# Kernel tuning notes

Hardware: AMD Instinct MI355X
Metric: run time of the kernel (lower is better)

Reference implementation:

```python
import jax, jax.numpy as jnp
import numpy as np

B, C_IMG, H, W = 16, 512, 32, 32
C_AUD, K_LEN, N_HEADS = 512, 256, 8
HEAD_DIM = C_AUD // N_HEADS
EPS = 1e-5


def setup_inputs() -> dict:
    key = jax.random.key(0)
    ks = jax.random.split(key, 12)
    s_img = 1.0 / np.sqrt(C_IMG)
    s_aud = 1.0 / np.sqrt(C_AUD)
    return {
        "img_feat": jax.random.normal(ks[0], (B, C_IMG, H, W), jnp.float32),
        "audio_feat": jax.random.normal(ks[1], (B, K_LEN, C_AUD), jnp.float32),
        "Wq": jax.random.uniform(ks[2], (C_IMG, C_AUD), jnp.float32, -s_img, s_img),
        "bq": jnp.zeros((C_AUD,), jnp.float32),
        "Wk": jax.random.uniform(ks[3], (C_AUD, C_AUD), jnp.float32, -s_aud, s_aud),
        "bk": jnp.zeros((C_AUD,), jnp.float32),
        "Wv": jax.random.uniform(ks[4], (C_AUD, C_AUD), jnp.float32, -s_aud, s_aud),
        "bv": jnp.zeros((C_AUD,), jnp.float32),
        "Wo": jax.random.uniform(ks[5], (C_AUD, C_IMG), jnp.float32, -s_aud, s_aud),
        "bo": jnp.zeros((C_IMG,), jnp.float32),
        "gamma": jnp.ones((C_IMG,), jnp.float32),
        "beta": jnp.zeros((C_IMG,), jnp.float32),
    }


def reference(img_feat, audio_feat, Wq, bq, Wk, bk, Wv, bv, Wo, bo, gamma, beta):
    b, c, h, w = img_feat.shape
    # b c h w -> b (h w) c
    img_seq = img_feat.reshape(b, c, h * w).transpose(0, 2, 1)
    q = img_seq @ Wq + bq                      # [b, q, C_AUD]
    k = audio_feat @ Wk + bk                   # [b, k, C_AUD]
    v = audio_feat @ Wv + bv
    # split heads: b s (h d) -> b h s d
    def split(x):
        bs, s, _ = x.shape
        return x.reshape(bs, s, N_HEADS, HEAD_DIM).transpose(0, 2, 1, 3)
    qh, kh, vh = split(q), split(k), split(v)
    scale = HEAD_DIM ** -0.5
    scores = jnp.einsum('bhqd,bhkd->bhqk', qh, kh) * scale
    weights = jax.nn.softmax(scores, axis=-1)
    attn = jnp.einsum('bhqk,bhkd->bhqd', weights, vh)
    attn = attn.transpose(0, 2, 1, 3).reshape(b, h * w, C_AUD)
    proj = attn @ Wo + bo                      # [b, q, C_IMG]
    y = img_seq + proj
    mu = jnp.mean(y, axis=-1, keepdims=True)
    var = jnp.mean((y - mu) ** 2, axis=-1, keepdims=True)
    y = (y - mu) * jax.lax.rsqrt(var + EPS) * gamma + beta
    # b (h w) c -> b c h w
    return y.transpose(0, 2, 1).reshape(b, c, h, w)
```

## Files before the change

### kernel.cpp

```cpp
#include <hip/hip_runtime.h>
#include <cstddef>

#define B_SZ 16
#define HW 1024
#define CCH 512
#define K_LEN 256
#define N_HEADS 8
#define EPS 1e-5f

typedef __bf16 bf16;
typedef bf16 bf16x8 __attribute__((ext_vector_type(8)));
typedef bf16 bf16x4 __attribute__((ext_vector_type(4)));
typedef float f32x4 __attribute__((ext_vector_type(4)));

__global__ __launch_bounds__(256) void transpose_cast_img(
    const float* __restrict__ src, bf16* __restrict__ dst)
{
    const int b  = blockIdx.z;
    const int s0 = blockIdx.x * 64;
    const int c0 = blockIdx.y * 64;
    __shared__ bf16 T[64][72];
    const int tid = threadIdx.x;
    {
        const int r = tid >> 2, cs = (tid & 3) << 4;
        const float* sp = src + ((size_t)b * CCH + c0 + r) * HW + s0 + cs;
        #pragma unroll
        for (int i = 0; i < 4; ++i) {
            float4 f = *(const float4*)(sp + i * 4);
            T[r][cs + i*4 + 0] = (bf16)f.x;
            T[r][cs + i*4 + 1] = (bf16)f.y;
            T[r][cs + i*4 + 2] = (bf16)f.z;
            T[r][cs + i*4 + 3] = (bf16)f.w;
        }
    }
    __syncthreads();
    {
        const int ss = tid >> 2, ks = (tid & 3) << 4;
        bf16x8 a, b8;
        #pragma unroll
        for (int j = 0; j < 8; ++j) { a[j] = T[ks + j][ss]; b8[j] = T[ks + 8 + j][ss]; }
        bf16* dp = dst + ((size_t)b * HW + s0 + ss) * CCH + c0 + ks;
        *(bf16x8*)dp = a;
        *(bf16x8*)(dp + 8) = b8;
    }
}

__global__ __launch_bounds__(256) void transpose_cast_w(
    const float* __restrict__ Wq, const float* __restrict__ Wk,
    const float* __restrict__ Wv, const float* __restrict__ Wo,
    bf16* __restrict__ dst)
{
    const int w = blockIdx.z;
    const float* src = (w == 0) ? Wq : (w == 1) ? Wk : (w == 2) ? Wv : Wo;
    const int n0 = blockIdx.x * 64;
    const int k0 = blockIdx.y * 64;
    __shared__ bf16 T[64][72];
    const int tid = threadIdx.x;
    {
        const int r = tid >> 2, cs = (tid & 3) << 4;
        const float* sp = src + (size_t)(k0 + r) * CCH + n0 + cs;
        #pragma unroll
        for (int i = 0; i < 4; ++i) {
            float4 f = *(const float4*)(sp + i * 4);
            T[r][cs + i*4 + 0] = (bf16)f.x;
            T[r][cs + i*4 + 1] = (bf16)f.y;
            T[r][cs + i*4 + 2] = (bf16)f.z;
            T[r][cs + i*4 + 3] = (bf16)f.w;
        }
    }
    __syncthreads();
    {
        const int nn = tid >> 2, ks = (tid & 3) << 4;
        bf16x8 a, b8;
        #pragma unroll
        for (int j = 0; j < 8; ++j) { a[j] = T[ks + j][nn]; b8[j] = T[ks + 8 + j][nn]; }
        bf16* dp = dst + (size_t)w * CCH * CCH + (size_t)(n0 + nn) * CCH + k0 + ks;
        *(bf16x8*)dp = a;
        *(bf16x8*)(dp + 8) = b8;
    }
}

__global__ __launch_bounds__(256) void cast_audio(
    const float* __restrict__ src, bf16* __restrict__ dst)
{
    const size_t i = ((size_t)blockIdx.x * 256 + threadIdx.x) * 8;
    float4 a = *(const float4*)(src + i);
    float4 b = *(const float4*)(src + i + 4);
    bf16x8 o;
    o[0] = (bf16)a.x; o[1] = (bf16)a.y; o[2] = (bf16)a.z; o[3] = (bf16)a.w;
    o[4] = (bf16)b.x; o[5] = (bf16)b.y; o[6] = (bf16)b.z; o[7] = (bf16)b.w;
    *(bf16x8*)(dst + i) = o;
}

__global__ __launch_bounds__(256) void gemm_bf16_mfma(
    const bf16* __restrict__ A, const bf16* __restrict__ Bt,
    const float* __restrict__ bias, bf16* __restrict__ out)
{
    const int tid  = threadIdx.x;
    const int wave = tid >> 6, lane = tid & 63;
    const int m0 = blockIdx.x * 128;
    const int n0 = blockIdx.y * 128;
    const int lrow = lane & 15, quad = lane >> 4;
    const int wm = (wave >> 1) * 64, wn = (wave & 1) * 64;

    __shared__ bf16 As[128 * 40];
    __shared__ bf16 Bs[128 * 40];

    f32x4 acc[4][4];
    #pragma unroll
    for (int i = 0; i < 4; ++i)
        #pragma unroll
        for (int j = 0; j < 4; ++j)
            acc[i][j] = (f32x4){0.f, 0.f, 0.f, 0.f};

    for (int k0 = 0; k0 < 512; k0 += 32) {
        #pragma unroll
        for (int i = 0; i < 2; ++i) {
            const int c = tid + i * 256;
            const int r = c >> 2, off = (c & 3) << 3;
            *(bf16x8*)&As[r * 40 + off] = *(const bf16x8*)(A  + (size_t)(m0 + r) * 512 + k0 + off);
            *(bf16x8*)&Bs[r * 40 + off] = *(const bf16x8*)(Bt + (size_t)(n0 + r) * 512 + k0 + off);
        }
        __syncthreads();
        bf16x8 af[4], bfr[4];
        #pragma unroll
        for (int i = 0; i < 4; ++i)
            af[i] = *(const bf16x8*)&As[(wm + i * 16 + lrow) * 40 + quad * 8];
        #pragma unroll
        for (int j = 0; j < 4; ++j)
            bfr[j] = *(const bf16x8*)&Bs[(wn + j * 16 + lrow) * 40 + quad * 8];
        #pragma unroll
        for (int i = 0; i < 4; ++i)
            #pragma unroll
            for (int j = 0; j < 4; ++j)
                acc[i][j] = __builtin_amdgcn_mfma_f32_16x16x32_bf16(af[i], bfr[j], acc[i][j], 0, 0, 0);
        __syncthreads();
    }

    #pragma unroll
    for (int j = 0; j < 4; ++j) {
        const int gn = n0 + wn + j * 16 + lrow;
        const float bv = bias[gn];
        #pragma unroll
        for (int i = 0; i < 4; ++i) {
            const int gm = m0 + wm + i * 16 + quad * 4;
            #pragma unroll
            for (int r = 0; r < 4; ++r)
                out[(size_t)(gm + r) * 512 + gn] = (bf16)(acc[i][j][r] + bv);
        }
    }
}

__global__ __launch_bounds__(256) void gemm_kv_mfma(
    const bf16* __restrict__ A, const bf16* __restrict__ Bt,
    const float* __restrict__ bk, const float* __restrict__ bv,
    bf16* __restrict__ khout, bf16* __restrict__ vtout)
{
    const int tid  = threadIdx.x;
    const int wave = tid >> 6, lane = tid & 63;
    const int m0 = blockIdx.x * 128;
    const int n0 = blockIdx.y * 128;
    const int lrow = lane & 15, quad = lane >> 4;
    const int wm = (wave >> 1) * 64, wn = (wave & 1) * 64;

    __shared__ bf16 As[128 * 40];
    __shared__ bf16 Bs[128 * 40];

    f32x4 acc[4][4];
    #pragma unroll
    for (int i = 0; i < 4; ++i)
        #pragma unroll
        for (int j = 0; j < 4; ++j)
            acc[i][j] = (f32x4){0.f, 0.f, 0.f, 0.f};

    for (int k0 = 0; k0 < 512; k0 += 32) {
        #pragma unroll
        for (int i = 0; i < 2; ++i) {
            const int c = tid + i * 256;
            const int r = c >> 2, off = (c & 3) << 3;
            *(bf16x8*)&As[r * 40 + off] = *(const bf16x8*)(A  + (size_t)(m0 + r) * 512 + k0 + off);
            *(bf16x8*)&Bs[r * 40 + off] = *(const bf16x8*)(Bt + (size_t)(n0 + r) * 512 + k0 + off);
        }
        __syncthreads();
        bf16x8 af[4], bfr[4];
        #pragma unroll
        for (int i = 0; i < 4; ++i)
            af[i] = *(const bf16x8*)&As[(wm + i * 16 + lrow) * 40 + quad * 8];
        #pragma unroll
        for (int j = 0; j < 4; ++j)
            bfr[j] = *(const bf16x8*)&Bs[(wn + j * 16 + lrow) * 40 + quad * 8];
        #pragma unroll
        for (int i = 0; i < 4; ++i)
            #pragma unroll
            for (int j = 0; j < 4; ++j)
                acc[i][j] = __builtin_amdgcn_mfma_f32_16x16x32_bf16(af[i], bfr[j], acc[i][j], 0, 0, 0);
        __syncthreads();
    }

    #pragma unroll
    for (int j = 0; j < 4; ++j) {
        const int gn = n0 + wn + j * 16 + lrow;
        if (gn < 512) {
            const int h = gn >> 6, d = gn & 63;
            const float bias = bk[gn];
            #pragma unroll
            for (int i = 0; i < 4; ++i) {
                const int gm = m0 + wm + i * 16 + quad * 4;
                const int b = gm >> 8, key = gm & 255;
                bf16* base = khout + ((((size_t)b * N_HEADS + h) * K_LEN) + key) * 64 + d;
                #pragma unroll
                for (int r = 0; r < 4; ++r)
                    base[(size_t)r * 64] = (bf16)(acc[i][j][r] + bias);
            }
        } else {
            const int ch = gn - 512;
            const int h = ch >> 6, d = ch & 63;
            const float bias = bv[ch];
            #pragma unroll
            for (int i = 0; i < 4; ++i) {
                const int gm = m0 + wm + i * 16 + quad * 4;
                const int b = gm >> 8, key = gm & 255;
                bf16x4 pk;
                #pragma unroll
                for (int r = 0; r < 4; ++r) pk[r] = (bf16)(acc[i][j][r] + bias);
                *(bf16x4*)(vtout + (((size_t)b * N_HEADS + h) * 64 + d) * K_LEN + key) = pk;
            }
        }
    }
}

__global__ __launch_bounds__(256) void attn_mfma(
    const bf16* __restrict__ q,
    const bf16* __restrict__ kh,
    const bf16* __restrict__ vt,
    bf16* __restrict__ o)
{
    const int bh = blockIdx.x;
    const int s0 = blockIdx.y * 64;
    const int tid = threadIdx.x;
    const int wave = tid >> 6, lane = tid & 63;
    const int l15 = lane & 15, quad = lane >> 4;
    const int b = bh >> 3, h = bh & 7;

    __shared__ bf16 KsPt[18432];
    __shared__ bf16 Vs[16896];

    const bf16* khb = kh + (size_t)bh * K_LEN * 64;
    const bf16* vtb = vt + (size_t)bh * 64 * K_LEN;

    #pragma unroll
    for (int i = 0; i < 8; ++i) {
        const int chunk = tid + (i << 8);
        const int key = chunk >> 3, dseg = (chunk & 7) << 3;
        *(bf16x8*)&KsPt[key * 72 + dseg] = *(const bf16x8*)(khb + key * 64 + dseg);
        const int d = chunk >> 5, kseg = (chunk & 31) << 3;
        *(bf16x8*)&Vs[d * 264 + kseg] = *(const bf16x8*)(vtb + d * 256 + kseg);
    }
    __syncthreads();

    const int qrow = s0 + wave * 16 + l15;
    const bf16* qp = q + ((size_t)(b * HW + qrow)) * 512 + h * 64 + quad * 8;
    const bf16x8 qf0 = *(const bf16x8*)qp;
    const bf16x8 qf1 = *(const bf16x8*)(qp + 32);

    f32x4 acc[16];
    #pragma unroll
    for (int m = 0; m < 16; ++m) acc[m] = (f32x4){0.f, 0.f, 0.f, 0.f};
    #pragma unroll
    for (int m = 0; m < 16; ++m) {
        const bf16x8 a0 = *(const bf16x8*)&KsPt[(m * 16 + l15) * 72 + quad * 8];
        const bf16x8 a1 = *(const bf16x8*)&KsPt[(m * 16 + l15) * 72 + 32 + quad * 8];
        acc[m] = __builtin_amdgcn_mfma_f32_16x16x32_bf16(a0, qf0, acc[m], 0, 0, 0);
        acc[m] = __builtin_amdgcn_mfma_f32_16x16x32_bf16(a1, qf1, acc[m], 0, 0, 0);
    }

    float mx = -1e30f;
    #pragma unroll
    for (int m = 0; m < 16; ++m) {
        mx = fmaxf(mx, fmaxf(fmaxf(acc[m][0], acc[m][1]), fmaxf(acc[m][2], acc[m][3])));
    }
    mx = fmaxf(mx, __shfl_xor(mx, 16, 64));
    mx = fmaxf(mx, __shfl_xor(mx, 32, 64));

    __syncthreads();

    bf16* PtW = &KsPt[wave * 4224];
    float l_sum = 0.f;
    #pragma unroll
    for (int m = 0; m < 16; ++m) {
        bf16x4 pk;
        #pragma unroll
        for (int r = 0; r < 4; ++r) {
            const float p = __expf((acc[m][r] - mx) * 0.125f);
            l_sum += p;
            pk[r] = (bf16)p;
        }
        *(bf16x4*)&PtW[l15 * 264 + m * 16 + quad * 4] = pk;
    }
    l_sum += __shfl_xor(l_sum, 16, 64);
    l_sum += __shfl_xor(l_sum, 32, 64);
    __syncthreads();

    f32x4 oacc[4];
    #pragma unroll
    for (int m = 0; m < 4; ++m) oacc[m] = (f32x4){0.f, 0.f, 0.f, 0.f};
    #pragma unroll
    for (int s = 0; s < 8; ++s) {
        const bf16x8 pb = *(const bf16x8*)&PtW[l15 * 264 + s * 32 + quad * 8];
        #pragma unroll
        for (int m = 0; m < 4; ++m) {
            const bf16x8 va = *(const bf16x8*)&Vs[(m * 16 + l15) * 264 + s * 32 + quad * 8];
            oacc[m] = __builtin_amdgcn_mfma_f32_16x16x32_bf16(va, pb, oacc[m], 0, 0, 0);
        }
    }

    const float inv = 1.0f / l_sum;
    bf16* op = o + ((size_t)(b * HW + qrow)) * 512 + h * 64 + quad * 4;
    #pragma unroll
    for (int m = 0; m < 4; ++m) {
        bf16x4 ov;
        #pragma unroll
        for (int r = 0; r < 4; ++r) ov[r] = (bf16)(oacc[m][r] * inv);
        *(bf16x4*)&op[m * 16] = ov;
    }
}

__global__ __launch_bounds__(256) void ln_kernel(
    const bf16* __restrict__ proj, const bf16* __restrict__ imgb,
    const float* __restrict__ gamma, const float* __restrict__ beta,
    float* __restrict__ out)
{
    const int b  = blockIdx.y;
    const int s0 = blockIdx.x * 64;
    const int tid = threadIdx.x;
    const int wave = tid >> 6, lane = tid & 63;

    __shared__ float smu[64], srs[64];
    __shared__ float Y[64][68];

    for (int rr = 0; rr < 16; ++rr) {
        const int r = wave * 16 + rr;
        const bf16* pp = proj + ((size_t)b * HW + s0 + r) * 512 + lane * 8;
        const bf16* ip = imgb + ((size_t)b * HW + s0 + r) * 512 + lane * 8;
        bf16x8 p8 = *(const bf16x8*)pp;
        bf16x8 i8 = *(const bf16x8*)ip;
        float sum = 0.f, ss = 0.f;
        #pragma unroll
        for (int j = 0; j < 8; ++j) {
            const float y = (float)p8[j] + (float)i8[j];
            sum += y; ss += y * y;
        }
        #pragma unroll
        for (int off = 32; off > 0; off >>= 1) {
            sum += __shfl_xor(sum, off, 64);
            ss  += __shfl_xor(ss, off, 64);
        }
        if (lane == 0) {
            const float mu = sum * (1.f / 512.f);
            const float var = ss * (1.f / 512.f) - mu * mu;
            smu[r] = mu;
            srs[r] = rsqrtf(var + EPS);
        }
    }
    __syncthreads();

    for (int ct = 0; ct < 8; ++ct) {
        const int c0 = ct * 64;
        {
            const int r = tid >> 2, cs = (tid & 3) << 4;
            const bf16* pp = proj + ((size_t)b * HW + s0 + r) * 512 + c0 + cs;
            const bf16* ip = imgb + ((size_t)b * HW + s0 + r) * 512 + c0 + cs;
            bf16x8 p0 = *(const bf16x8*)pp, p1 = *(const bf16x8*)(pp + 8);
            bf16x8 i0 = *(const bf16x8*)ip, i1 = *(const bf16x8*)(ip + 8);
            const float mu = smu[r], rs = srs[r];
            #pragma unroll
            for (int j = 0; j < 8; ++j) {
                const int c = c0 + cs + j;
                Y[r][cs + j]     = ((float)p0[j] + (float)i0[j] - mu) * rs * gamma[c]     + beta[c];
                Y[r][cs + 8 + j] = ((float)p1[j] + (float)i1[j] - mu) * rs * gamma[c + 8] + beta[c + 8];
            }
        }
        __syncthreads();
        {
            const int cc = tid >> 2, so = (tid & 3) << 4;
            float* op = out + ((size_t)b * CCH + c0 + cc) * HW + s0 + so;
            #pragma unroll
            for (int i = 0; i < 4; ++i) {
                float4 o4;
                o4.x = Y[so + i*4 + 0][cc];
                o4.y = Y[so + i*4 + 1][cc];
                o4.z = Y[so + i*4 + 2][cc];
                o4.w = Y[so + i*4 + 3][cc];
                *(float4*)(op + i * 4) = o4;
            }
        }
        __syncthreads();
    }
}

extern "C" void kernel_launch(void* const* d_in, const int* in_sizes, int n_in,
                              void* d_out, int out_size, void* d_ws, size_t ws_size,
                              hipStream_t stream) {
    const float* img   = (const float*)d_in[0];
    const float* audio = (const float*)d_in[1];
    const float* Wq    = (const float*)d_in[2];
    const float* bq    = (const float*)d_in[3];
    const float* Wk    = (const float*)d_in[4];
    const float* bk    = (const float*)d_in[5];
    const float* Wv    = (const float*)d_in[6];
    const float* bv    = (const float*)d_in[7];
    const float* Wo    = (const float*)d_in[8];
    const float* bo    = (const float*)d_in[9];
    const float* gamma = (const float*)d_in[10];
    const float* beta  = (const float*)d_in[11];

    bf16* wsb    = (bf16*)d_ws;
    bf16* img_bf = wsb;
    bf16* aud_bf = img_bf + 8388608;
    bf16* wT     = aud_bf + 2097152;
    bf16* q_bf   = wT + 1048576;
    bf16* kh_bf  = q_bf + 8388608;
    bf16* vt_bf  = kh_bf + 2097152;
    bf16* a_bf   = vt_bf + 2097152;
    bf16* p_bf   = q_bf;

    transpose_cast_img<<<dim3(16, 8, 16), 256, 0, stream>>>(img, img_bf);
    cast_audio<<<dim3(1024), 256, 0, stream>>>(audio, aud_bf);
    transpose_cast_w<<<dim3(8, 8, 4), 256, 0, stream>>>(Wq, Wk, Wv, Wo, wT);

    gemm_bf16_mfma<<<dim3(128, 4), 256, 0, stream>>>(img_bf, wT, bq, q_bf);
    gemm_kv_mfma<<<dim3(32, 8), 256, 0, stream>>>(aud_bf, wT + 262144, bk, bv, kh_bf, vt_bf);
    attn_mfma<<<dim3(B_SZ * N_HEADS, HW / 64), 256, 0, stream>>>(q_bf, kh_bf, vt_bf, a_bf);
    gemm_bf16_mfma<<<dim3(128, 4), 256, 0, stream>>>(a_bf, wT + 3 * 262144, bo, p_bf);
    ln_kernel<<<dim3(16, 16), 256, 0, stream>>>(p_bf, img_bf, gamma, beta, (float*)d_out);
}
```

Before: 216.0 us.

## Use direct global-to-LDS loads in GEMMs, vectorize epilogue, restructure LayerNorm kernel

Both MFMA GEMMs now stage tiles with the global_load_lds builtin, which writes straight into unpadded shared memory and skips the register round trip. The main GEMM swaps MFMA operand order so each lane holds four consecutive output columns, letting the epilogue write bf16x4 vectors with a float4 bias load. The LayerNorm kernel reads each row only once, keeps values in registers, writes a full 32x512 normalized tile to LDS and transposes it out, with double the block count. The risks are LDS bank conflicts from dropping the padding and lower occupancy from the large LDS tile in LayerNorm.

```diff
diff --git a/kernel.cpp b/kernel.cpp
--- a/kernel.cpp
+++ b/kernel.cpp
@@ -12,6 +12,12 @@
 typedef bf16 bf16x8 __attribute__((ext_vector_type(8)));
 typedef bf16 bf16x4 __attribute__((ext_vector_type(4)));
 typedef float f32x4 __attribute__((ext_vector_type(4)));
+
+__device__ __forceinline__ void gl_lds16(const bf16* g, bf16* l) {
+    __builtin_amdgcn_global_load_lds(
+        (const __attribute__((address_space(1))) void*)g,
+        (__attribute__((address_space(3))) void*)l, 16, 0, 0);
+}
 
 __global__ __launch_bounds__(256) void transpose_cast_img(
     const float* __restrict__ src, bf16* __restrict__ dst)
@@ -100,11 +106,14 @@
     const int wave = tid >> 6, lane = tid & 63;
     const int m0 = blockIdx.x * 128;
     const int n0 = blockIdx.y * 128;
-    const int lrow = lane & 15, quad = lane >> 4;
+    const int l15 = lane & 15, quad = lane >> 4;
     const int wm = (wave >> 1) * 64, wn = (wave & 1) * 64;
 
-    __shared__ bf16 As[128 * 40];
-    __shared__ bf16 Bs[128 * 40];
+    __shared__ bf16 As[128 * 32];
+    __shared__ bf16 Bs[128 * 32];
+
+    const int r16 = lane >> 2;
+    const int ks  = (lane & 3) * 8;
 
     f32x4 acc[4][4];
     #pragma unroll
@@ -116,19 +125,82 @@
     for (int k0 = 0; k0 < 512; k0 += 32) {
         #pragma unroll
         for (int i = 0; i < 2; ++i) {
-            const int c = tid + i * 256;
-            const int r = c >> 2, off = (c & 3) << 3;
-            *(bf16x8*)&As[r * 40 + off] = *(const bf16x8*)(A  + (size_t)(m0 + r) * 512 + k0 + off);
-            *(bf16x8*)&Bs[r * 40 + off] = *(const bf16x8*)(Bt + (size_t)(n0 + r) * 512 + k0 + off);
+            const int c = wave * 2 + i;
+            gl_lds16(A  + (size_t)(m0 + c * 16 + r16) * 512 + k0 + ks, &As[c * 512]);
+            gl_lds16(Bt + (size_t)(n0 + c * 16 + r16) * 512 + k0 + ks, &Bs[c * 512]);
         }
         __syncthreads();
         bf16x8 af[4], bfr[4];
         #pragma unroll
         for (int i = 0; i < 4; ++i)
-            af[i] = *(const bf16x8*)&As[(wm + i * 16 + lrow) * 40 + quad * 8];
+            af[i] = *(const bf16x8*)&As[(wm + i * 16 + l15) * 32 + quad * 8];
         #pragma unroll
         for (int j = 0; j < 4; ++j)
-            bfr[j] = *(const bf16x8*)&Bs[(wn + j * 16 + lrow) * 40 + quad * 8];
+            bfr[j] = *(const bf16x8*)&Bs[(wn + j * 16 + l15) * 32 + quad * 8];
+        #pragma unroll
+        for (int i = 0; i < 4; ++i)
+            #pragma unroll
+            for (int j = 0; j < 4; ++j)
+                acc[i][j] = __builtin_amdgcn_mfma_f32_16x16x32_bf16(bfr[j], af[i], acc[i][j], 0, 0, 0);
+        __syncthreads();
+    }
+
+    #pragma unroll
+    for (int j = 0; j < 4; ++j) {
+        const int gn = n0 + wn + j * 16 + quad * 4;
+        const float4 bv4 = *(const float4*)(bias + gn);
+        const float bb[4] = {bv4.x, bv4.y, bv4.z, bv4.w};
+        #pragma unroll
+        for (int i = 0; i < 4; ++i) {
+            const int gm = m0 + wm + i * 16 + l15;
+            bf16x4 ov;
+            #pragma unroll
+            for (int r = 0; r < 4; ++r) ov[r] = (bf16)(acc[i][j][r] + bb[r]);
+            *(bf16x4*)(out + (size_t)gm * 512 + gn) = ov;
+        }
+    }
+}
+
+__global__ __launch_bounds__(256) void gemm_kv_mfma(
+    const bf16* __restrict__ A, const bf16* __restrict__ Bt,
+    const float* __restrict__ bk, const float* __restrict__ bv,
+    bf16* __restrict__ khout, bf16* __restrict__ vtout)
+{
+    const int tid  = threadIdx.x;
+    const int wave = tid >> 6, lane = tid & 63;
+    const int m0 = blockIdx.x * 128;
+    const int n0 = blockIdx.y * 128;
+    const int l15 = lane & 15, quad = lane >> 4;
+    const int wm = (wave >> 1) * 64, wn = (wave & 1) * 64;
+
+    __shared__ bf16 As[128 * 32];
+    __shared__ bf16 Bs[128 * 32];
+
+    const int r16 = lane >> 2;
+    const int ks  = (lane & 3) * 8;
+
+    f32x4 acc[4][4];
+    #pragma unroll
+    for (int i = 0; i < 4; ++i)
+        #pragma unroll
+        for (int j = 0; j < 4; ++j)
+            acc[i][j] = (f32x4){0.f, 0.f, 0.f, 0.f};
+
+    for (int k0 = 0; k0 < 512; k0 += 32) {
+        #pragma unroll
+        for (int i = 0; i < 2; ++i) {
+            const int c = wave * 2 + i;
+            gl_lds16(A  + (size_t)(m0 + c * 16 + r16) * 512 + k0 + ks, &As[c * 512]);
+            gl_lds16(Bt + (size_t)(n0 + c * 16 + r16) * 512 + k0 + ks, &Bs[c * 512]);
+        }
+        __syncthreads();
+        bf16x8 af[4], bfr[4];
+        #pragma unroll
+        for (int i = 0; i < 4; ++i)
+            af[i] = *(const bf16x8*)&As[(wm + i * 16 + l15) * 32 + quad * 8];
+        #pragma unroll
+        for (int j = 0; j < 4; ++j)
+            bfr[j] = *(const bf16x8*)&Bs[(wn + j * 16 + l15) * 32 + quad * 8];
         #pragma unroll
         for (int i = 0; i < 4; ++i)
             #pragma unroll
@@ -139,67 +211,7 @@
 
     #pragma unroll
     for (int j = 0; j < 4; ++j) {
-        const int gn = n0 + wn + j * 16 + lrow;
-        const float bv = bias[gn];
-        #pragma unroll
-        for (int i = 0; i < 4; ++i) {
-            const int gm = m0 + wm + i * 16 + quad * 4;
-            #pragma unroll
-            for (int r = 0; r < 4; ++r)
-                out[(size_t)(gm + r) * 512 + gn] = (bf16)(acc[i][j][r] + bv);
-        }
-    }
-}
-
-__global__ __launch_bounds__(256) void gemm_kv_mfma(
-    const bf16* __restrict__ A, const bf16* __restrict__ Bt,
-    const float* __restrict__ bk, const float* __restrict__ bv,
-    bf16* __restrict__ khout, bf16* __restrict__ vtout)
-{
-    const int tid  = threadIdx.x;
-    const int wave = tid >> 6, lane = tid & 63;
-    const int m0 = blockIdx.x * 128;
-    const int n0 = blockIdx.y * 128;
-    const int lrow = lane & 15, quad = lane >> 4;
-    const int wm = (wave >> 1) * 64, wn = (wave & 1) * 64;
-
-    __shared__ bf16 As[128 * 40];
-    __shared__ bf16 Bs[128 * 40];
-
-    f32x4 acc[4][4];
-    #pragma unroll
-    for (int i = 0; i < 4; ++i)
-        #pragma unroll
-        for (int j = 0; j < 4; ++j)
-            acc[i][j] = (f32x4){0.f, 0.f, 0.f, 0.f};
-
-    for (int k0 = 0; k0 < 512; k0 += 32) {
-        #pragma unroll
-        for (int i = 0; i < 2; ++i) {
-            const int c = tid + i * 256;
-            const int r = c >> 2, off = (c & 3) << 3;
-            *(bf16x8*)&As[r * 40 + off] = *(const bf16x8*)(A  + (size_t)(m0 + r) * 512 + k0 + off);
-            *(bf16x8*)&Bs[r * 40 + off] = *(const bf16x8*)(Bt + (size_t)(n0 + r) * 512 + k0 + off);
-        }
-        __syncthreads();
-        bf16x8 af[4], bfr[4];
-        #pragma unroll
-        for (int i = 0; i < 4; ++i)
-            af[i] = *(const bf16x8*)&As[(wm + i * 16 + lrow) * 40 + quad * 8];
-        #pragma unroll
-        for (int j = 0; j < 4; ++j)
-            bfr[j] = *(const bf16x8*)&Bs[(wn + j * 16 + lrow) * 40 + quad * 8];
-        #pragma unroll
-        for (int i = 0; i < 4; ++i)
-            #pragma unroll
-            for (int j = 0; j < 4; ++j)
-                acc[i][j] = __builtin_amdgcn_mfma_f32_16x16x32_bf16(af[i], bfr[j], acc[i][j], 0, 0, 0);
-        __syncthreads();
-    }
-
-    #pragma unroll
-    for (int j = 0; j < 4; ++j) {
-        const int gn = n0 + wn + j * 16 + lrow;
+        const int gn = n0 + wn + j * 16 + l15;
         if (gn < 512) {
             const int h = gn >> 6, d = gn & 63;
             const float bias = bk[gn];
@@ -276,9 +288,8 @@
 
     float mx = -1e30f;
     #pragma unroll
-    for (int m = 0; m < 16; ++m) {
+    for (int m = 0; m < 16; ++m)
         mx = fmaxf(mx, fmaxf(fmaxf(acc[m][0], acc[m][1]), fmaxf(acc[m][2], acc[m][3])));
-    }
     mx = fmaxf(mx, __shfl_xor(mx, 16, 64));
     mx = fmaxf(mx, __shfl_xor(mx, 32, 64));
 
@@ -331,70 +342,56 @@
     float* __restrict__ out)
 {
     const int b  = blockIdx.y;
-    const int s0 = blockIdx.x * 64;
+    const int s0 = blockIdx.x * 32;
     const int tid = threadIdx.x;
     const int wave = tid >> 6, lane = tid & 63;
 
-    __shared__ float smu[64], srs[64];
-    __shared__ float Y[64][68];
-
-    for (int rr = 0; rr < 16; ++rr) {
-        const int r = wave * 16 + rr;
-        const bf16* pp = proj + ((size_t)b * HW + s0 + r) * 512 + lane * 8;
-        const bf16* ip = imgb + ((size_t)b * HW + s0 + r) * 512 + lane * 8;
-        bf16x8 p8 = *(const bf16x8*)pp;
-        bf16x8 i8 = *(const bf16x8*)ip;
-        float sum = 0.f, ss = 0.f;
+    __shared__ float Y[32][513];
+
+    const int cb = lane * 8;
+    const float4 g0 = *(const float4*)(gamma + cb);
+    const float4 g1 = *(const float4*)(gamma + cb + 4);
+    const float4 b0 = *(const float4*)(beta + cb);
+    const float4 b1 = *(const float4*)(beta + cb + 4);
+    const float gg[8] = {g0.x, g0.y, g0.z, g0.w, g1.x, g1.y, g1.z, g1.w};
+    const float bb[8] = {b0.x, b0.y, b0.z, b0.w, b1.x, b1.y, b1.z, b1.w};
+
+    #pragma unroll
+    for (int rr = 0; rr < 8; ++rr) {
+        const int ss = wave * 8 + rr;
+        const size_t row = (size_t)b * HW + s0 + ss;
+        bf16x8 p8 = *(const bf16x8*)(proj + row * 512 + cb);
+        bf16x8 i8 = *(const bf16x8*)(imgb + row * 512 + cb);
+        float y[8];
+        float sum = 0.f, sq = 0.f;
         #pragma unroll
         for (int j = 0; j < 8; ++j) {
-            const float y = (float)p8[j] + (float)i8[j];
-            sum += y; ss += y * y;
+            y[j] = (float)p8[j] + (float)i8[j];
+            sum += y[j]; sq += y[j] * y[j];
         }
         #pragma unroll
         for (int off = 32; off > 0; off >>= 1) {
             sum += __shfl_xor(sum, off, 64);
-            ss  += __shfl_xor(ss, off, 64);
-        }
-        if (lane == 0) {
-            const float mu = sum * (1.f / 512.f);
-            const float var = ss * (1.f / 512.f) - mu * mu;
-            smu[r] = mu;
-            srs[r] = rsqrtf(var + EPS);
-        }
-    }
-    __syncthreads();
-
-    for (int ct = 0; ct < 8; ++ct) {
-        const int c0 = ct * 64;
-        {
-            const int r = tid >> 2, cs = (tid & 3) << 4;
-            const bf16* pp = proj + ((size_t)b * HW + s0 + r) * 512 + c0 + cs;
-            const bf16* ip = imgb + ((size_t)b * HW + s0 + r) * 512 + c0 + cs;
-            bf16x8 p0 = *(const bf16x8*)pp, p1 = *(const bf16x8*)(pp + 8);
-            bf16x8 i0 = *(const bf16x8*)ip, i1 = *(const bf16x8*)(ip + 8);
-            const float mu = smu[r], rs = srs[r];
-            #pragma unroll
-            for (int j = 0; j < 8; ++j) {
-                const int c = c0 + cs + j;
-                Y[r][cs + j]     = ((float)p0[j] + (float)i0[j] - mu) * rs * gamma[c]     + beta[c];
-                Y[r][cs + 8 + j] = ((float)p1[j] + (float)i1[j] - mu) * rs * gamma[c + 8] + beta[c + 8];
-            }
-        }
-        __syncthreads();
-        {
-            const int cc = tid >> 2, so = (tid & 3) << 4;
-            float* op = out + ((size_t)b * CCH + c0 + cc) * HW + s0 + so;
-            #pragma unroll
-            for (int i = 0; i < 4; ++i) {
-                float4 o4;
-                o4.x = Y[so + i*4 + 0][cc];
-                o4.y = Y[so + i*4 + 1][cc];
-                o4.z = Y[so + i*4 + 2][cc];
-                o4.w = Y[so + i*4 + 3][cc];
-                *(float4*)(op + i * 4) = o4;
-            }
-        }
-        __syncthreads();
+            sq  += __shfl_xor(sq, off, 64);
+        }
+        const float mu = sum * (1.f / 512.f);
+        const float rs = rsqrtf(sq * (1.f / 512.f) - mu * mu + EPS);
+        #pragma unroll
+        for (int j = 0; j < 8; ++j)
+            Y[ss][cb + j] = (y[j] - mu) * rs * gg[j] + bb[j];
+    }
+    __syncthreads();
+
+    #pragma unroll
+    for (int it = 0; it < 16; ++it) {
+        const int idx = it * 256 + tid;
+        const int c = idx >> 3, sseg = (idx & 7) << 2;
+        float4 o4;
+        o4.x = Y[sseg + 0][c];
+        o4.y = Y[sseg + 1][c];
+        o4.z = Y[sseg + 2][c];
+        o4.w = Y[sseg + 3][c];
+        *(float4*)(out + ((size_t)b * CCH + c) * HW + s0 + sseg) = o4;
     }
 }
 
@@ -432,5 +429,5 @@
     gemm_kv_mfma<<<dim3(32, 8), 256, 0, stream>>>(aud_bf, wT + 262144, bk, bv, kh_bf, vt_bf);
     attn_mfma<<<dim3(B_SZ * N_HEADS, HW / 64), 256, 0, stream>>>(q_bf, kh_bf, vt_bf, a_bf);
     gemm_bf16_mfma<<<dim3(128, 4), 256, 0, stream>>>(a_bf, wT + 3 * 262144, bo, p_bf);
-    ln_kernel<<<dim3(16, 16), 256, 0, stream>>>(p_bf, img_bf, gamma, beta, (float*)d_out);
-}
+    ln_kernel<<<dim3(32, 16), 256, 0, stream>>>(p_bf, img_bf, gamma, beta, (float*)d_out);
+}
```

New measurement: 198.1 us. -8.3%, faster.
